# Optimization experiments

Hardware: AMD Instinct MI355X
Metric: run time of the kernel (lower is better)

Reference implementation:

```python
import jax, jax.numpy as jnp
import numpy as np

B, H, S, D = 2, 8, 2048, 64
WINDOW = 3            # local_attention_window (default in torch forward)
FRAC = 0.3            # percentage_frac hardcoded in create_window_tensor call
MASK_FILL = -1.0e9


def window_kernel(window, frac):
    # create_window_tensor: [ (1-f)^n ... (1-f)^1, 1, (1-f)^1 ... (1-f)^n ]
    n = (window - 1) // 2
    side = np.array([(1.0 - frac) ** i for i in range(n, 0, -1)], dtype=np.float32)
    vals = np.concatenate([side, np.array([1.0], np.float32), side[::-1]])
    return jnp.asarray(vals)


def setup_inputs() -> dict:
    key = jax.random.key(0)
    kq, kk, kv = jax.random.split(key, 3)
    queries = jax.random.normal(kq, (B, H, S, D), jnp.float32)
    keys = jax.random.normal(kk, (B, H, S, D), jnp.float32)
    values = jax.random.normal(kv, (B, H, S, D), jnp.float32)
    # causal mask: True positions are filled with -1e9 (masked_fill semantics)
    mask = jnp.triu(jnp.ones((S, S), dtype=bool), 1)[None, None]  # [1,1,S,S]
    # linear_bias: nn.Parameter(torch.zeros(Sk)) created inside forward
    beta = jnp.zeros((S,), jnp.float32)
    return {"queries": queries, "keys": keys, "values": values,
            "beta": beta, "mask": mask}


def reference(queries, keys, values, beta, mask):
    d = keys.shape[-1]
    # scores = Q K^T / sqrt(d)
    scores = jnp.einsum("bhqd,bhkd->bhqk", queries, keys) / jnp.sqrt(
        jnp.asarray(d, queries.dtype))
    scores = jnp.where(mask, jnp.asarray(MASK_FILL, scores.dtype), scores)
    # include_local_attention=True, local_attention_dim_vertical=False:
    # the torch code transposes, conv2d with a [1,W] kernel along the last
    # axis, transposes back -> 1D cross-correlation along the QUERY axis.
    # Kernel is symmetric so correlation == convolution. Zero padding.
    kern = window_kernel(WINDOW, FRAC)
    p = (WINDOW - 1) // 2
    xp = jnp.pad(scores, ((0, 0), (0, 0), (p, p), (0, 0)))
    Sq = scores.shape[2]
    scores = sum(kern[i] * jax.lax.dynamic_slice_in_dim(xp, i, Sq, axis=2)
                 for i in range(WINDOW))
    # linear_bias=True: add zero-initialized per-key-position bias
    scores = scores + beta  # broadcasts over last dim [Sk]
    weights = jax.nn.softmax(scores, axis=-1)
    return jnp.einsum("bhqk,bhkd->bhqd", weights, values)
```

## Files before the change

### kernel.cpp

```cpp
#include <hip/hip_runtime.h>


typedef short bf16x8 __attribute__((ext_vector_type(8)));
typedef float f32x4  __attribute__((ext_vector_type(4)));

constexpr int S_ = 2048;
constexpr int D_ = 64;
constexpr float LOG2E = 1.44269504088896341f;
constexpr float KSC = 0.125f * LOG2E;

__device__ __forceinline__ unsigned pk2(float lo, float hi) {
    union { float f; unsigned u; } a, b;
    a.f = lo; b.f = hi;
    return __builtin_amdgcn_perm(b.u + 0x8000u, a.u + 0x8000u, 0x07060302u);
}

__global__ __launch_bounds__(256)
void cvt_k(const float* __restrict__ K, unsigned short* __restrict__ Kbf)
{
    const size_t i = ((size_t)blockIdx.x * 256 + threadIdx.x) * 8;
    float4 a = *(const float4*)(K + i);
    float4 b = *(const float4*)(K + i + 4);
    *(uint4*)(Kbf + i) = make_uint4(pk2(a.x, a.y), pk2(a.z, a.w),
                                    pk2(b.x, b.y), pk2(b.z, b.w));
}

__global__ __launch_bounds__(256)
void cvt_v(const float* __restrict__ V, unsigned short* __restrict__ Vt)
{
    __shared__ float T[64][65];
    const int k0 = blockIdx.x << 6;
    const int hd = blockIdx.y;
    const int t = threadIdx.x;
    {
        const int ky = t >> 2, dc = (t & 3) << 4;
        const float* vp = V + (((size_t)hd * S_) + k0 + ky) * D_ + dc;
        #pragma unroll
        for (int i = 0; i < 4; ++i) {
            float4 v4 = *(const float4*)(vp + 4 * i);
            T[ky][dc + 4 * i + 0] = v4.x;
            T[ky][dc + 4 * i + 1] = v4.y;
            T[ky][dc + 4 * i + 2] = v4.z;
            T[ky][dc + 4 * i + 3] = v4.w;
        }
    }
    __syncthreads();
    {
        const int d = t >> 2, kc = (t & 3) << 4;
        unsigned w[8];
        #pragma unroll
        for (int j = 0; j < 8; ++j)
            w[j] = pk2(T[kc + 2 * j][d], T[kc + 2 * j + 1][d]);
        unsigned short* op = Vt + ((size_t)hd * D_ + d) * S_ + k0 + kc;
        *(uint4*)(op)     = make_uint4(w[0], w[1], w[2], w[3]);
        *(uint4*)(op + 8) = make_uint4(w[4], w[5], w[6], w[7]);
    }
}

__global__ __launch_bounds__(256, 2)
void attn6(const float* __restrict__ Q, const float* __restrict__ beta,
           const unsigned short* __restrict__ Kbf, const unsigned short* __restrict__ Vt,
           float* __restrict__ out)
{
    __shared__ float opub[2][32][68];
    __shared__ float lred[2][32];

    const int bid = blockIdx.x;
    const int hd = bid & 15;
    const int pr = bid >> 4;

    const float* Qh = Q + (size_t)hd * S_ * D_;
    const unsigned short* Kh = Kbf + (size_t)hd * S_ * D_;
    const unsigned short* Vh = Vt + (size_t)hd * D_ * S_;

    const int t = threadIdx.x, lane = t & 63;
    const int wv = t >> 6, kh = wv & 1, sg = wv >> 1;
    const int n_l = lane & 15, qd = lane >> 4;
    const int qdo = qd << 3;

    int krow[2];
    krow[0] = (kh << 5) + ((n_l >> 2) << 3) + (n_l & 3);
    krow[1] = krow[0] + 4;
    int dmb[4];
    #pragma unroll
    for (int mb = 0; mb < 4; ++mb) dmb[mb] = (mb << 4) + n_l;
    const int kvo = (kh << 5) + qdo;

    for (int p = 0; p < 2; ++p) {
        const int j = p ? (31 - pr) : pr;
        const int q0 = j << 6;
        const int nt = j + 1;
        const int qbase = q0 + (sg << 5);

        auto ld = [&](int tile, bf16x8 (&ka)[2][2], bf16x8 (&vb)[4], float (&bt)[8]) {
            const unsigned short* kp = Kh + (size_t)(tile << 6) * D_;
            #pragma unroll
            for (int mb = 0; mb < 2; ++mb)
                #pragma unroll
                for (int hh = 0; hh < 2; ++hh)
                    ka[mb][hh] = *(const bf16x8*)(kp + krow[mb] * D_ + (hh << 5) + qdo);
            const unsigned short* vp = Vh + (tile << 6) + kvo;
            #pragma unroll
            for (int mb = 0; mb < 4; ++mb)
                vb[mb] = *(const bf16x8*)(vp + (size_t)dmb[mb] * S_);
            const float* bp = beta + (tile << 6) + kvo;
            float4 b0 = *(const float4*)(bp);
            float4 b1 = *(const float4*)(bp + 4);
            bt[0] = b0.x * LOG2E; bt[1] = b0.y * LOG2E;
            bt[2] = b0.z * LOG2E; bt[3] = b0.w * LOG2E;
            bt[4] = b1.x * LOG2E; bt[5] = b1.y * LOG2E;
            bt[6] = b1.z * LOG2E; bt[7] = b1.w * LOG2E;
        };

        bf16x8 kaA[2][2], vbA[4]; float btA[8];
        bf16x8 kaB[2][2], vbB[4]; float btB[8];
        ld(0, kaA, vbA, btA);

        bf16x8 qb[2][2];
        #pragma unroll
        for (int ng = 0; ng < 2; ++ng) {
            const int q = qbase + (ng << 4) + n_l;
            const float wp = (q > 0) ? 0.7f : 0.0f;
            const float wn = (q + 1 < S_) ? 0.7f : 0.0f;
            const float* qc = Qh + (size_t)q * D_;
            const float* qpp = qc - ((q > 0) ? D_ : 0);
            const float* qnn = qc + ((q + 1 < S_) ? D_ : 0);
            #pragma unroll
            for (int hh = 0; hh < 2; ++hh) {
                const int d0 = (hh << 5) + qdo;
                float4 c0 = *(const float4*)(qc + d0),  c1 = *(const float4*)(qc + d0 + 4);
                float4 p0 = *(const float4*)(qpp + d0), p1 = *(const float4*)(qpp + d0 + 4);
                float4 n0 = *(const float4*)(qnn + d0), n1 = *(const float4*)(qnn + d0 + 4);
                float e0 = fmaf(wn, n0.x, fmaf(wp, p0.x, c0.x));
                float e1 = fmaf(wn, n0.y, fmaf(wp, p0.y, c0.y));
                float e2 = fmaf(wn, n0.z, fmaf(wp, p0.z, c0.z));
                float e3 = fmaf(wn, n0.w, fmaf(wp, p0.w, c0.w));
                float e4 = fmaf(wn, n1.x, fmaf(wp, p1.x, c1.x));
                float e5 = fmaf(wn, n1.y, fmaf(wp, p1.y, c1.y));
                float e6 = fmaf(wn, n1.z, fmaf(wp, p1.z, c1.z));
                float e7 = fmaf(wn, n1.w, fmaf(wp, p1.w, c1.w));
                union { unsigned u[4]; bf16x8 v; } qu;
                qu.u[0] = pk2(e0, e1); qu.u[1] = pk2(e2, e3);
                qu.u[2] = pk2(e4, e5); qu.u[3] = pk2(e6, e7);
                qb[ng][hh] = qu.v;
            }
        }

        f32x4 o[4][2];
        float l[2] = {0.0f, 0.0f};
        #pragma unroll
        for (int mb = 0; mb < 4; ++mb)
            #pragma unroll
            for (int ng = 0; ng < 2; ++ng) o[mb][ng] = (f32x4){0, 0, 0, 0};

        auto comp = [&](int tile, bf16x8 (&ka)[2][2], bf16x8 (&vb)[4], float (&bt)[8]) {
            const f32x4 zz = {0, 0, 0, 0};
            f32x4 acc[2][2];
            #pragma unroll
            for (int mb = 0; mb < 2; ++mb)
                #pragma unroll
                for (int ng = 0; ng < 2; ++ng) {
                    f32x4 a = __builtin_amdgcn_mfma_f32_16x16x32_bf16(ka[mb][0], qb[ng][0], zz, 0, 0, 0);
                    acc[mb][ng] = __builtin_amdgcn_mfma_f32_16x16x32_bf16(ka[mb][1], qb[ng][1], a, 0, 0, 0);
                }
            const bool dm = (tile == nt - 1);
            const int kk = (tile << 6) + kvo;
            union { unsigned u[4]; bf16x8 v; } pf[2];
            #pragma unroll
            for (int ng = 0; ng < 2; ++ng) {
                const int qr = qbase + (ng << 4) + n_l;
                float pv[8];
                float la = 0.0f;
                #pragma unroll
                for (int jj = 0; jj < 8; ++jj) {
                    const int mb = jj >> 2, r = jj & 3;
                    float sv = fmaf(acc[mb][ng][r], KSC, bt[jj]);
                    if (dm) {
                        const int key = kk + jj;
                        if (!((key < qr) || (qr == 0 && key == 0))) sv = -1.0e30f;
                    }
                    pv[jj] = __builtin_amdgcn_exp2f(sv);
                    la += pv[jj];
                }
                l[ng] += la;
                pf[ng].u[0] = pk2(pv[0], pv[1]);
                pf[ng].u[1] = pk2(pv[2], pv[3]);
                pf[ng].u[2] = pk2(pv[4], pv[5]);
                pf[ng].u[3] = pk2(pv[6], pv[7]);
            }
            #pragma unroll
            for (int mb = 0; mb < 4; ++mb)
                #pragma unroll
                for (int ng = 0; ng < 2; ++ng)
                    o[mb][ng] = __builtin_amdgcn_mfma_f32_16x16x32_bf16(vb[mb], pf[ng].v, o[mb][ng], 0, 0, 0);
        };

        int it = 0;
        for (; it + 2 <= nt; it += 2) {
            ld(it + 1, kaB, vbB, btB);
            comp(it, kaA, vbA, btA);
            if (it + 2 < nt) ld(it + 2, kaA, vbA, btA);
            comp(it + 1, kaB, vbB, btB);
        }
        if (it < nt) comp(it, kaA, vbA, btA);

        #pragma unroll
        for (int ng = 0; ng < 2; ++ng) {
            l[ng] += __shfl_xor(l[ng], 16);
            l[ng] += __shfl_xor(l[ng], 32);
        }
        __syncthreads();
        if (kh == 0) {
            #pragma unroll
            for (int ng = 0; ng < 2; ++ng) {
                const int row = (ng << 4) + n_l;
                #pragma unroll
                for (int mb = 0; mb < 4; ++mb)
                    *(float4*)&opub[sg][row][(mb << 4) + (qd << 2)] =
                        make_float4(o[mb][ng][0], o[mb][ng][1], o[mb][ng][2], o[mb][ng][3]);
                if (qd == 0) lred[sg][row] = l[ng];
            }
        }
        __syncthreads();
        if (kh == 1) {
            #pragma unroll
            for (int ng = 0; ng < 2; ++ng) {
                const int row = (ng << 4) + n_l;
                const float inv = 1.0f / (l[ng] + lred[sg][row]);
                float* op = out + ((size_t)hd * S_ + qbase + row) * D_ + (qd << 2);
                #pragma unroll
                for (int mb = 0; mb < 4; ++mb) {
                    float4 pv = *(float4*)&opub[sg][row][(mb << 4) + (qd << 2)];
                    *(float4*)(op + (mb << 4)) =
                        make_float4((o[mb][ng][0] + pv.x) * inv, (o[mb][ng][1] + pv.y) * inv,
                                    (o[mb][ng][2] + pv.z) * inv, (o[mb][ng][3] + pv.w) * inv);
                }
            }
        }
    }
}

extern "C" void kernel_launch(void* const* d_in, const int* in_sizes, int n_in,
                              void* d_out, int out_size, void* d_ws, size_t ws_size,
                              hipStream_t stream) {
    const float* Q    = (const float*)d_in[0];
    const float* K    = (const float*)d_in[1];
    const float* V    = (const float*)d_in[2];
    const float* beta = (const float*)d_in[3];
    float* out = (float*)d_out;

    unsigned short* Kbf = (unsigned short*)d_ws;
    unsigned short* Vt  = Kbf + (size_t)16 * S_ * D_;

    cvt_k<<<dim3(1024), 256, 0, stream>>>(K, Kbf);
    cvt_v<<<dim3(32, 16), 256, 0, stream>>>(V, Vt);
    attn6<<<dim3(256), 256, 0, stream>>>(Q, beta, Kbf, Vt, out);
}
```

Before: 128.2 us.

## Pre-swizzle K/V into MFMA fragment layout and use 8 waves per block

Replaces the separate K bf16 conversion and V transpose kernels with one kernel that writes K and V directly in per-lane MFMA fragment order, so the attention kernel does fully contiguous 16-byte loads per lane. The attention kernel now uses 512 threads with each wave handling 16 query rows instead of 32, which halves per-wave accumulators and raises wave count for latency hiding. The prefetch is reordered to keep two tiles in flight. The trade-off is that each wave does less MFMA work per K/V load, so K/V fragment traffic per block doubles, and the V gather in the convert kernel uses strided scalar reads.

New measurement: 118.0 us. 1.09x faster.

```diff
diff --git a/kernel.cpp b/kernel.cpp
--- a/kernel.cpp
+++ b/kernel.cpp
@@ -16,96 +16,90 @@
 }
 
 __global__ __launch_bounds__(256)
-void cvt_k(const float* __restrict__ K, unsigned short* __restrict__ Kbf)
+void cvt_frag(const float* __restrict__ K, const float* __restrict__ V,
+              unsigned short* __restrict__ F)
 {
-    const size_t i = ((size_t)blockIdx.x * 256 + threadIdx.x) * 8;
-    float4 a = *(const float4*)(K + i);
-    float4 b = *(const float4*)(K + i + 4);
-    *(uint4*)(Kbf + i) = make_uint4(pk2(a.x, a.y), pk2(a.z, a.w),
-                                    pk2(b.x, b.y), pk2(b.z, b.w));
-}
-
-__global__ __launch_bounds__(256)
-void cvt_v(const float* __restrict__ V, unsigned short* __restrict__ Vt)
+    const int tid  = blockIdx.x * 256 + threadIdx.x;
+    const int lane = tid & 63;
+    const int frag = (tid >> 6) & 15;
+    const int tt   = (tid >> 10) & 31;
+    const int hd   = tid >> 15;
+    const int n_l = lane & 15, qd = lane >> 4;
+    unsigned w[4];
+    if (frag < 8) {
+        const int kh = frag >> 2, mb = (frag >> 1) & 1, hh = frag & 1;
+        const int key = tt * 64 + kh * 32 + ((n_l >> 2) << 3) + (n_l & 3) + mb * 4;
+        const int d0  = hh * 32 + qd * 8;
+        const float* src = K + (size_t)(hd * S_ + key) * D_ + d0;
+        float4 a = *(const float4*)src;
+        float4 b = *(const float4*)(src + 4);
+        w[0] = pk2(a.x, a.y); w[1] = pk2(a.z, a.w);
+        w[2] = pk2(b.x, b.y); w[3] = pk2(b.z, b.w);
+    } else {
+        const int kh = (frag >> 2) & 1, mb = frag & 3;
+        const int key0 = tt * 64 + kh * 32 + qd * 8;
+        const int d = mb * 16 + n_l;
+        const float* src = V + (size_t)(hd * S_ + key0) * D_ + d;
+        float e[8];
+        #pragma unroll
+        for (int j = 0; j < 8; ++j) e[j] = src[j * D_];
+        w[0] = pk2(e[0], e[1]); w[1] = pk2(e[2], e[3]);
+        w[2] = pk2(e[4], e[5]); w[3] = pk2(e[6], e[7]);
+    }
+    *(uint4*)(F + (size_t)tid * 8) = make_uint4(w[0], w[1], w[2], w[3]);
+}
+
+__global__ __launch_bounds__(512, 2)
+void attn7(const float* __restrict__ Q, const float* __restrict__ beta,
+           const unsigned short* __restrict__ F, float* __restrict__ out)
 {
-    __shared__ float T[64][65];
-    const int k0 = blockIdx.x << 6;
-    const int hd = blockIdx.y;
-    const int t = threadIdx.x;
-    {
-        const int ky = t >> 2, dc = (t & 3) << 4;
-        const float* vp = V + (((size_t)hd * S_) + k0 + ky) * D_ + dc;
-        #pragma unroll
-        for (int i = 0; i < 4; ++i) {
-            float4 v4 = *(const float4*)(vp + 4 * i);
-            T[ky][dc + 4 * i + 0] = v4.x;
-            T[ky][dc + 4 * i + 1] = v4.y;
-            T[ky][dc + 4 * i + 2] = v4.z;
-            T[ky][dc + 4 * i + 3] = v4.w;
-        }
-    }
-    __syncthreads();
-    {
-        const int d = t >> 2, kc = (t & 3) << 4;
-        unsigned w[8];
-        #pragma unroll
-        for (int j = 0; j < 8; ++j)
-            w[j] = pk2(T[kc + 2 * j][d], T[kc + 2 * j + 1][d]);
-        unsigned short* op = Vt + ((size_t)hd * D_ + d) * S_ + k0 + kc;
-        *(uint4*)(op)     = make_uint4(w[0], w[1], w[2], w[3]);
-        *(uint4*)(op + 8) = make_uint4(w[4], w[5], w[6], w[7]);
-    }
-}
-
-__global__ __launch_bounds__(256, 2)
-void attn6(const float* __restrict__ Q, const float* __restrict__ beta,
-           const unsigned short* __restrict__ Kbf, const unsigned short* __restrict__ Vt,
-           float* __restrict__ out)
-{
-    __shared__ float opub[2][32][68];
-    __shared__ float lred[2][32];
+    __shared__ float opub[4][16][68];
+    __shared__ float lred[4][16];
 
     const int bid = blockIdx.x;
     const int hd = bid & 15;
     const int pr = bid >> 4;
 
     const float* Qh = Q + (size_t)hd * S_ * D_;
-    const unsigned short* Kh = Kbf + (size_t)hd * S_ * D_;
-    const unsigned short* Vh = Vt + (size_t)hd * D_ * S_;
+    const unsigned short* Fh = F + (size_t)hd * 32 * 16 * 512;
 
     const int t = threadIdx.x, lane = t & 63;
     const int wv = t >> 6, kh = wv & 1, sg = wv >> 1;
     const int n_l = lane & 15, qd = lane >> 4;
-    const int qdo = qd << 3;
-
-    int krow[2];
-    krow[0] = (kh << 5) + ((n_l >> 2) << 3) + (n_l & 3);
-    krow[1] = krow[0] + 4;
-    int dmb[4];
+
+    const int lo = lane * 8;
+    int kfo[2][2], vfo[4];
     #pragma unroll
-    for (int mb = 0; mb < 4; ++mb) dmb[mb] = (mb << 4) + n_l;
-    const int kvo = (kh << 5) + qdo;
+    for (int mb = 0; mb < 2; ++mb)
+        #pragma unroll
+        for (int hh = 0; hh < 2; ++hh)
+            kfo[mb][hh] = ((kh << 2) | (mb << 1) | hh) * 512 + lo;
+    #pragma unroll
+    for (int mb = 0; mb < 4; ++mb)
+        vfo[mb] = (8 + (kh << 2) + mb) * 512 + lo;
+
+    const int kvo = (kh << 5) + (qd << 3);
+    const float* bp = beta + kvo;
 
     for (int p = 0; p < 2; ++p) {
         const int j = p ? (31 - pr) : pr;
         const int q0 = j << 6;
         const int nt = j + 1;
-        const int qbase = q0 + (sg << 5);
+        const int qbase = q0 + (sg << 4);
+        const int qr = qbase + n_l;
 
         auto ld = [&](int tile, bf16x8 (&ka)[2][2], bf16x8 (&vb)[4], float (&bt)[8]) {
-            const unsigned short* kp = Kh + (size_t)(tile << 6) * D_;
-            #pragma unroll
-            for (int mb = 0; mb < 2; ++mb)
-                #pragma unroll
-                for (int hh = 0; hh < 2; ++hh)
-                    ka[mb][hh] = *(const bf16x8*)(kp + krow[mb] * D_ + (hh << 5) + qdo);
-            const unsigned short* vp = Vh + (tile << 6) + kvo;
+            const unsigned short* fp = Fh + (size_t)tile * 8192;
+            ka[0][0] = *(const bf16x8*)(fp + kfo[0][0]);
+            ka[0][1] = *(const bf16x8*)(fp + kfo[0][1]);
+            ka[1][0] = *(const bf16x8*)(fp + kfo[1][0]);
+            ka[1][1] = *(const bf16x8*)(fp + kfo[1][1]);
             #pragma unroll
             for (int mb = 0; mb < 4; ++mb)
-                vb[mb] = *(const bf16x8*)(vp + (size_t)dmb[mb] * S_);
-            const float* bp = beta + (tile << 6) + kvo;
-            float4 b0 = *(const float4*)(bp);
-            float4 b1 = *(const float4*)(bp + 4);
+                vb[mb] = *(const bf16x8*)(fp + vfo[mb]);
+            const float* bq = bp + (tile << 6);
+            float4 b0 = *(const float4*)(bq);
+            float4 b1 = *(const float4*)(bq + 4);
             bt[0] = b0.x * LOG2E; bt[1] = b0.y * LOG2E;
             bt[2] = b0.z * LOG2E; bt[3] = b0.w * LOG2E;
             bt[4] = b1.x * LOG2E; bt[5] = b1.y * LOG2E;
@@ -115,19 +109,18 @@
         bf16x8 kaA[2][2], vbA[4]; float btA[8];
         bf16x8 kaB[2][2], vbB[4]; float btB[8];
         ld(0, kaA, vbA, btA);
-
-        bf16x8 qb[2][2];
-        #pragma unroll
-        for (int ng = 0; ng < 2; ++ng) {
-            const int q = qbase + (ng << 4) + n_l;
-            const float wp = (q > 0) ? 0.7f : 0.0f;
-            const float wn = (q + 1 < S_) ? 0.7f : 0.0f;
-            const float* qc = Qh + (size_t)q * D_;
-            const float* qpp = qc - ((q > 0) ? D_ : 0);
-            const float* qnn = qc + ((q + 1 < S_) ? D_ : 0);
+        if (nt > 1) ld(1, kaB, vbB, btB);
+
+        bf16x8 qb[2];
+        {
+            const float wp = (qr > 0) ? 0.7f : 0.0f;
+            const float wn = (qr + 1 < S_) ? 0.7f : 0.0f;
+            const float* qc = Qh + (size_t)qr * D_;
+            const float* qpp = qc - ((qr > 0) ? D_ : 0);
+            const float* qnn = qc + ((qr + 1 < S_) ? D_ : 0);
             #pragma unroll
             for (int hh = 0; hh < 2; ++hh) {
-                const int d0 = (hh << 5) + qdo;
+                const int d0 = (hh << 5) + (qd << 3);
                 float4 c0 = *(const float4*)(qc + d0),  c1 = *(const float4*)(qc + d0 + 4);
                 float4 p0 = *(const float4*)(qpp + d0), p1 = *(const float4*)(qpp + d0 + 4);
                 float4 n0 = *(const float4*)(qnn + d0), n1 = *(const float4*)(qnn + d0 + 4);
@@ -142,99 +135,78 @@
                 union { unsigned u[4]; bf16x8 v; } qu;
                 qu.u[0] = pk2(e0, e1); qu.u[1] = pk2(e2, e3);
                 qu.u[2] = pk2(e4, e5); qu.u[3] = pk2(e6, e7);
-                qb[ng][hh] = qu.v;
-            }
-        }
-
-        f32x4 o[4][2];
-        float l[2] = {0.0f, 0.0f};
+                qb[hh] = qu.v;
+            }
+        }
+
+        f32x4 o[4];
+        float l = 0.0f;
         #pragma unroll
-        for (int mb = 0; mb < 4; ++mb)
-            #pragma unroll
-            for (int ng = 0; ng < 2; ++ng) o[mb][ng] = (f32x4){0, 0, 0, 0};
+        for (int mb = 0; mb < 4; ++mb) o[mb] = (f32x4){0, 0, 0, 0};
 
         auto comp = [&](int tile, bf16x8 (&ka)[2][2], bf16x8 (&vb)[4], float (&bt)[8]) {
             const f32x4 zz = {0, 0, 0, 0};
-            f32x4 acc[2][2];
-            #pragma unroll
-            for (int mb = 0; mb < 2; ++mb)
-                #pragma unroll
-                for (int ng = 0; ng < 2; ++ng) {
-                    f32x4 a = __builtin_amdgcn_mfma_f32_16x16x32_bf16(ka[mb][0], qb[ng][0], zz, 0, 0, 0);
-                    acc[mb][ng] = __builtin_amdgcn_mfma_f32_16x16x32_bf16(ka[mb][1], qb[ng][1], a, 0, 0, 0);
-                }
+            f32x4 acc[2];
+            #pragma unroll
+            for (int mb = 0; mb < 2; ++mb) {
+                f32x4 a = __builtin_amdgcn_mfma_f32_16x16x32_bf16(ka[mb][0], qb[0], zz, 0, 0, 0);
+                acc[mb] = __builtin_amdgcn_mfma_f32_16x16x32_bf16(ka[mb][1], qb[1], a, 0, 0, 0);
+            }
             const bool dm = (tile == nt - 1);
             const int kk = (tile << 6) + kvo;
-            union { unsigned u[4]; bf16x8 v; } pf[2];
-            #pragma unroll
-            for (int ng = 0; ng < 2; ++ng) {
-                const int qr = qbase + (ng << 4) + n_l;
-                float pv[8];
-                float la = 0.0f;
-                #pragma unroll
-                for (int jj = 0; jj < 8; ++jj) {
-                    const int mb = jj >> 2, r = jj & 3;
-                    float sv = fmaf(acc[mb][ng][r], KSC, bt[jj]);
-                    if (dm) {
-                        const int key = kk + jj;
-                        if (!((key < qr) || (qr == 0 && key == 0))) sv = -1.0e30f;
-                    }
-                    pv[jj] = __builtin_amdgcn_exp2f(sv);
-                    la += pv[jj];
+            float pv[8];
+            float la = 0.0f;
+            #pragma unroll
+            for (int jj = 0; jj < 8; ++jj) {
+                const int mb = jj >> 2, r = jj & 3;
+                float sv = fmaf(acc[mb][r], KSC, bt[jj]);
+                if (dm) {
+                    const int key = kk + jj;
+                    if (!((key < qr) || (qr == 0 && key == 0))) sv = -1.0e30f;
                 }
-                l[ng] += la;
-                pf[ng].u[0] = pk2(pv[0], pv[1]);
-                pf[ng].u[1] = pk2(pv[2], pv[3]);
-                pf[ng].u[2] = pk2(pv[4], pv[5]);
-                pf[ng].u[3] = pk2(pv[6], pv[7]);
-            }
+                pv[jj] = __builtin_amdgcn_exp2f(sv);
+                la += pv[jj];
+            }
+            l += la;
+            union { unsigned u[4]; bf16x8 v; } pf;
+            pf.u[0] = pk2(pv[0], pv[1]);
+            pf.u[1] = pk2(pv[2], pv[3]);
+            pf.u[2] = pk2(pv[4], pv[5]);
+            pf.u[3] = pk2(pv[6], pv[7]);
             #pragma unroll
             for (int mb = 0; mb < 4; ++mb)
-                #pragma unroll
-                for (int ng = 0; ng < 2; ++ng)
-                    o[mb][ng] = __builtin_amdgcn_mfma_f32_16x16x32_bf16(vb[mb], pf[ng].v, o[mb][ng], 0, 0, 0);
+                o[mb] = __builtin_amdgcn_mfma_f32_16x16x32_bf16(vb[mb], pf.v, o[mb], 0, 0, 0);
         };
 
         int it = 0;
         for (; it + 2 <= nt; it += 2) {
-            ld(it + 1, kaB, vbB, btB);
             comp(it, kaA, vbA, btA);
             if (it + 2 < nt) ld(it + 2, kaA, vbA, btA);
             comp(it + 1, kaB, vbB, btB);
+            if (it + 3 < nt) ld(it + 3, kaB, vbB, btB);
         }
         if (it < nt) comp(it, kaA, vbA, btA);
 
-        #pragma unroll
-        for (int ng = 0; ng < 2; ++ng) {
-            l[ng] += __shfl_xor(l[ng], 16);
-            l[ng] += __shfl_xor(l[ng], 32);
-        }
+        l += __shfl_xor(l, 16);
+        l += __shfl_xor(l, 32);
         __syncthreads();
         if (kh == 0) {
             #pragma unroll
-            for (int ng = 0; ng < 2; ++ng) {
-                const int row = (ng << 4) + n_l;
-                #pragma unroll
-                for (int mb = 0; mb < 4; ++mb)
-                    *(float4*)&opub[sg][row][(mb << 4) + (qd << 2)] =
-                        make_float4(o[mb][ng][0], o[mb][ng][1], o[mb][ng][2], o[mb][ng][3]);
-                if (qd == 0) lred[sg][row] = l[ng];
-            }
+            for (int mb = 0; mb < 4; ++mb)
+                *(float4*)&opub[sg][n_l][(mb << 4) + (qd << 2)] =
+                    make_float4(o[mb][0], o[mb][1], o[mb][2], o[mb][3]);
+            if (qd == 0) lred[sg][n_l] = l;
         }
         __syncthreads();
         if (kh == 1) {
-            #pragma unroll
-            for (int ng = 0; ng < 2; ++ng) {
-                const int row = (ng << 4) + n_l;
-                const float inv = 1.0f / (l[ng] + lred[sg][row]);
-                float* op = out + ((size_t)hd * S_ + qbase + row) * D_ + (qd << 2);
-                #pragma unroll
-                for (int mb = 0; mb < 4; ++mb) {
-                    float4 pv = *(float4*)&opub[sg][row][(mb << 4) + (qd << 2)];
-                    *(float4*)(op + (mb << 4)) =
-                        make_float4((o[mb][ng][0] + pv.x) * inv, (o[mb][ng][1] + pv.y) * inv,
-                                    (o[mb][ng][2] + pv.z) * inv, (o[mb][ng][3] + pv.w) * inv);
-                }
+            const float inv = 1.0f / (l + lred[sg][n_l]);
+            float* op = out + ((size_t)hd * S_ + qr) * D_ + (qd << 2);
+            #pragma unroll
+            for (int mb = 0; mb < 4; ++mb) {
+                float4 pv = *(float4*)&opub[sg][n_l][(mb << 4) + (qd << 2)];
+                *(float4*)(op + (mb << 4)) =
+                    make_float4((o[mb][0] + pv.x) * inv, (o[mb][1] + pv.y) * inv,
+                                (o[mb][2] + pv.z) * inv, (o[mb][3] + pv.w) * inv);
             }
         }
     }
@@ -249,10 +221,8 @@
     const float* beta = (const float*)d_in[3];
     float* out = (float*)d_out;
 
-    unsigned short* Kbf = (unsigned short*)d_ws;
-    unsigned short* Vt  = Kbf + (size_t)16 * S_ * D_;
-
-    cvt_k<<<dim3(1024), 256, 0, stream>>>(K, Kbf);
-    cvt_v<<<dim3(32, 16), 256, 0, stream>>>(V, Vt);
-    attn6<<<dim3(256), 256, 0, stream>>>(Q, beta, Kbf, Vt, out);
-}
+    unsigned short* F = (unsigned short*)d_ws;
+
+    cvt_frag<<<dim3(2048), 256, 0, stream>>>(K, V, F);
+    attn7<<<dim3(256), 512, 0, stream>>>(Q, beta, F, out);
+}
```
